# Performance work log

Measured on AMD Instinct MI355X. Metric: run time of the kernel, lower is better.

The kernel has to match this reference:

```python
import jax, jax.numpy as jnp
import numpy as np

WS = 12
NUM_HEADS = 6
EPS = 1e-5


def _ln(x, w, b):
    mu = jnp.mean(x, axis=-1, keepdims=True)
    var = jnp.var(x, axis=-1, keepdims=True)
    return (x - mu) * jax.lax.rsqrt(var + EPS) * w + b


def _lin(x, w, b):
    return jnp.einsum('...i,oi->...o', x, w) + b


def _window_partition(x, ws):
    # x: [B, C, H, W] -> [B*Nh*Nw, ws*ws, C]
    B, C, H, W = x.shape
    x = x.reshape(B, C, H // ws, ws, W // ws, ws)
    x = jnp.transpose(x, (0, 2, 4, 3, 5, 1))
    return x.reshape(-1, ws * ws, C)


def _window_reverse(win, ws, B, C, H, W):
    Nh, Nw = H // ws, W // ws
    x = win.reshape(B, Nh, Nw, ws, ws, C)
    x = jnp.transpose(x, (0, 5, 1, 3, 2, 4))
    return x.reshape(B, C, H, W)


def setup_inputs() -> dict:
    key = jax.random.key(0)
    ks = jax.random.split(key, 12)
    B, C, H, W = 4, 192, 240, 240
    hid = 4 * C
    s = 0.02
    return {
        'opt': jax.random.normal(ks[0], (B, C, H, W), jnp.float32),
        'sar': jax.random.normal(ks[1], (B, C, H, W), jnp.float32),
        'ln_q_w': jnp.ones((C,), jnp.float32), 'ln_q_b': jnp.zeros((C,), jnp.float32),
        'ln_kv_w': jnp.ones((C,), jnp.float32), 'ln_kv_b': jnp.zeros((C,), jnp.float32),
        'wq': jax.random.normal(ks[2], (C, C), jnp.float32) * s, 'bq': jnp.zeros((C,), jnp.float32),
        'wk': jax.random.normal(ks[3], (C, C), jnp.float32) * s, 'bk': jnp.zeros((C,), jnp.float32),
        'wv': jax.random.normal(ks[4], (C, C), jnp.float32) * s, 'bv': jnp.zeros((C,), jnp.float32),
        'wp': jax.random.normal(ks[5], (C, C), jnp.float32) * s, 'bp': jnp.zeros((C,), jnp.float32),
        'gw1': jax.random.normal(ks[6], (C, C), jnp.float32) * s, 'gb1': jnp.zeros((C,), jnp.float32),
        'gw2': jax.random.normal(ks[7], (C, C), jnp.float32) * s, 'gb2': jnp.zeros((C,), jnp.float32),
        'gamma': jnp.float32(0.1),
        'ln_o_w': jnp.ones((C,), jnp.float32), 'ln_o_b': jnp.zeros((C,), jnp.float32),
        'w1': jax.random.normal(ks[8], (hid, C), jnp.float32) * s, 'b1': jnp.zeros((hid,), jnp.float32),
        'w2': jax.random.normal(ks[9], (C, hid), jnp.float32) * s, 'b2': jnp.zeros((C,), jnp.float32),
    }


def reference(opt, sar, ln_q_w, ln_q_b, ln_kv_w, ln_kv_b, wq, bq, wk, bk, wv, bv,
              wp, bp, gw1, gb1, gw2, gb2, gamma, ln_o_w, ln_o_b, w1, b1, w2, b2):
    B, C, H, W = opt.shape
    Hh = NUM_HEADS
    hd = C // Hh
    scale = hd ** -0.5

    opt_tok = _window_partition(opt, WS)   # [Bn, N, C]
    sar_tok = _window_partition(sar, WS)
    Bn, N, _ = opt_tok.shape

    opt_ln = _ln(opt_tok, ln_q_w, ln_q_b)
    sar_ln = _ln(sar_tok, ln_kv_w, ln_kv_b)

    q = _lin(opt_ln, wq, bq).reshape(Bn, N, Hh, hd)
    k = _lin(sar_ln, wk, bk).reshape(Bn, N, Hh, hd)
    v = _lin(sar_ln, wv, bv).reshape(Bn, N, Hh, hd)

    attn = jnp.einsum('bnhd,bmhd->bhnm', q, k) * scale
    attn = jax.nn.softmax(attn, axis=-1)
    out = jnp.einsum('bhnm,bmhd->bnhd', attn, v).reshape(Bn, N, C)
    fused = _lin(out, wp, bp)

    # sigmoid gate on mean-pooled sar tokens
    g = jax.nn.sigmoid(_lin(jax.nn.gelu(_lin(jnp.mean(sar_ln, axis=1), gw1, gb1), approximate=False), gw2, gb2))
    fused = opt_tok + gamma * (g[:, None, :] * fused)

    h = _ln(fused, ln_o_w, ln_o_b)
    h = _lin(jax.nn.gelu(_lin(h, w1, b1), approximate=False), w2, b2)
    fused = fused + h

    return _window_reverse(fused, WS, B, C, H, W)
```

## Files before the change

### kernel.cpp

```cpp
#include <hip/hip_runtime.h>
#include <hip/hip_bf16.h>

#define ROWS 230400
#define CDIM 192
#define NTOK 144
#define NWIN 1600
#define PLANE 57600
#define HDIM 768

typedef __attribute__((ext_vector_type(8))) short bf16x8;
typedef __attribute__((ext_vector_type(4))) float f32x4;

__device__ __forceinline__ ushort f2bf(float f) {
  union { float f; unsigned u; } v; v.f = f;
  unsigned r = v.u + 0x7FFFu + ((v.u >> 16) & 1u);
  return (ushort)(r >> 16);
}
__device__ __forceinline__ float bf2f(ushort h) {
  union { unsigned u; float f; } v; v.u = ((unsigned)h) << 16;
  return v.f;
}
__device__ __forceinline__ float gelu_f(float x) {
  return 0.5f * x * (1.f + erff(x * 0.7071067811865475f));
}

struct CvtJobs {
  const float* src[8];
  ushort* dst[8];
  int n[8];
};
__global__ __launch_bounds__(256) void cvt_kernel(CvtJobs jobs) {
  int stride = gridDim.x * blockDim.x;
  int t0 = blockIdx.x * blockDim.x + threadIdx.x;
  for (int j = 0; j < 8; ++j) {
    const float* s = jobs.src[j]; ushort* d = jobs.dst[j]; int n = jobs.n[j];
    for (int e = t0; e < n; e += stride) d[e] = f2bf(s[e]);
  }
}

__global__ __launch_bounds__(256) void lnpart_kernel(
    const float* __restrict__ opt, const float* __restrict__ sar,
    const float* __restrict__ lnqw, const float* __restrict__ lnqb,
    const float* __restrict__ lnkw, const float* __restrict__ lnkb,
    ushort* __restrict__ opt_ln, ushort* __restrict__ sar_ln,
    ushort* __restrict__ opt_tok) {
  __shared__ __align__(16) ushort X[NTOK * 200];
  __shared__ float smu[NTOK], srs[NTOK];
  int win = blockIdx.x;
  int b = win / 400, rr = win % 400, nh = rr / 20, nw = rr % 20;
  size_t wbase = (size_t)b * CDIM * PLANE + (size_t)(nh * 12) * 240 + nw * 12;
  int tid = threadIdx.x;
  for (int pass = 0; pass < 2; ++pass) {
    const float* src = pass ? sar : opt;
    for (int e = tid; e < CDIM * 36; e += 256) {
      int c = e / 36, r2 = e % 36, i = r2 / 3, j0 = (r2 % 3) * 4;
      float4 v = *(const float4*)&src[wbase + (size_t)c * PLANE + i * 240 + j0];
      int tok = i * 12 + j0;
      X[(tok + 0) * 200 + c] = f2bf(v.x);
      X[(tok + 1) * 200 + c] = f2bf(v.y);
      X[(tok + 2) * 200 + c] = f2bf(v.z);
      X[(tok + 3) * 200 + c] = f2bf(v.w);
    }
    __syncthreads();
    if (tid < NTOK) {
      float s = 0.f, qs = 0.f;
      for (int c = 0; c < CDIM; ++c) { float v = bf2f(X[tid * 200 + c]); s += v; qs += v * v; }
      float mu = s * (1.f / CDIM);
      smu[tid] = mu;
      srs[tid] = rsqrtf(qs * (1.f / CDIM) - mu * mu + 1e-5f);
    }
    __syncthreads();
    const float* w = pass ? lnkw : lnqw;
    const float* bb = pass ? lnkb : lnqb;
    ushort* dst = pass ? sar_ln : opt_ln;
    for (int e = tid; e < NTOK * CDIM; e += 256) {
      int tok = e / CDIM, c = e % CDIM;
      ushort raw = X[tok * 200 + c];
      float v = bf2f(raw);
      float y = (v - smu[tok]) * srs[tok] * w[c] + bb[c];
      size_t o = (size_t)(win * NTOK + tok) * CDIM + c;
      dst[o] = f2bf(y);
      if (!pass) opt_tok[o] = raw;
    }
    __syncthreads();
  }
}

enum { EPI_BF16 = 0, EPI_GELU = 1, EPI_SIG = 2, EPI_PROJ = 3 };

template <int EPI>
__global__ __launch_bounds__(256) void gemm_kernel(
    const ushort* __restrict__ A, const ushort* __restrict__ Wt,
    const float* __restrict__ bias, const float* __restrict__ bias2,
    void* __restrict__ outp, int M, int N, int K,
    const float* __restrict__ g, const ushort* __restrict__ opt_tok,
    const float* __restrict__ gamma_p) {
  __shared__ __align__(16) ushort Alds[128 * 40];
  int m0 = blockIdx.x * 128;
  int n0 = blockIdx.y * 64;
  int tid = threadIdx.x;
  int wave = tid >> 6, lane = tid & 63, ls = lane & 15, quad = lane >> 4;
  f32x4 acc[2][4] = {};
  for (int k0 = 0; k0 < K; k0 += 32) {
    for (int it = 0; it < 2; ++it) {
      int ch = tid + 256 * it;
      int r = ch >> 2, c8 = (ch & 3) * 8;
      int grow = m0 + r; if (grow > M - 1) grow = M - 1;
      *(bf16x8*)&Alds[r * 40 + c8] = *(const bf16x8*)&A[(size_t)grow * K + k0 + c8];
    }
    __syncthreads();
    int mb = wave * 32;
    bf16x8 af0 = *(const bf16x8*)&Alds[(mb + ls) * 40 + quad * 8];
    bf16x8 af1 = *(const bf16x8*)&Alds[(mb + 16 + ls) * 40 + quad * 8];
    bf16x8 bfr[4];
    for (int nf = 0; nf < 4; ++nf)
      bfr[nf] = *(const bf16x8*)&Wt[(size_t)(n0 + nf * 16 + ls) * K + k0 + quad * 8];
    for (int nf = 0; nf < 4; ++nf) {
      acc[0][nf] = __builtin_amdgcn_mfma_f32_16x16x32_bf16(af0, bfr[nf], acc[0][nf], 0, 0, 0);
      acc[1][nf] = __builtin_amdgcn_mfma_f32_16x16x32_bf16(af1, bfr[nf], acc[1][nf], 0, 0, 0);
    }
    __syncthreads();
  }
  float gam = (EPI == EPI_PROJ) ? gamma_p[0] : 0.f;
  for (int s = 0; s < 2; ++s) {
    int rowbase = m0 + wave * 32 + s * 16 + quad * 4;
    for (int nf = 0; nf < 4; ++nf) {
      int col = n0 + nf * 16 + ls;
      float bb = (col < 192) ? bias[col] : bias2[col - 192];
      for (int r = 0; r < 4; ++r) {
        int row = rowbase + r;
        if (row >= M) continue;
        float v = acc[s][nf][r] + bb;
        if (EPI == EPI_BF16) {
          ((ushort*)outp)[(size_t)row * N + col] = f2bf(v);
        } else if (EPI == EPI_GELU) {
          ((ushort*)outp)[(size_t)row * N + col] = f2bf(gelu_f(v));
        } else if (EPI == EPI_SIG) {
          ((float*)outp)[(size_t)row * N + col] = 1.f / (1.f + __expf(-v));
        } else {
          int win = row / NTOK;
          float gv = g[(size_t)win * CDIM + col];
          float ov = bf2f(opt_tok[(size_t)row * CDIM + col]);
          ((ushort*)outp)[(size_t)row * CDIM + col] = f2bf(ov + gam * gv * v);
        }
      }
    }
  }
}

__global__ __launch_bounds__(192) void pool_kernel(const ushort* __restrict__ sar_ln,
                                                   ushort* __restrict__ pool) {
  int win = blockIdx.x, c = threadIdx.x;
  float s = 0.f;
  size_t base = (size_t)win * NTOK * CDIM + c;
  for (int t = 0; t < NTOK; ++t) s += bf2f(sar_ln[base + (size_t)t * CDIM]);
  pool[(size_t)win * CDIM + c] = f2bf(s * (1.f / NTOK));
}

__global__ __launch_bounds__(256) void attn_kernel(const ushort* __restrict__ q,
                                                   const ushort* __restrict__ kv,
                                                   ushort* __restrict__ attn_out) {
  __shared__ __align__(16) ushort vT[32 * 168];
  __shared__ __align__(16) ushort P[4][16 * 168];
  int blk = blockIdx.x;
  int win = blk / 6, head = blk % 6;
  int tid = threadIdx.x, wave = tid >> 6, lane = tid & 63, ls = lane & 15, quad = lane >> 4;
  size_t qbase = (size_t)win * NTOK * CDIM + head * 32;
  size_t kbase = (size_t)win * NTOK * 384 + head * 32;
  size_t vbase = kbase + 192;
  for (int e = tid; e < NTOK * 32; e += 256) {
    int t = e >> 5, d = e & 31;
    vT[d * 168 + t] = kv[vbase + (size_t)t * 384 + d];
  }
  for (int e = tid; e < 32 * 24; e += 256) {
    int d = e / 24, j = 144 + e % 24;
    vT[d * 168 + j] = 0;
  }
  __syncthreads();
  const float scale = 0.17677669529663687f;
  ushort* Pw = P[wave];
  f32x4 zero = {0.f, 0.f, 0.f, 0.f};
  for (int mt = wave; mt < 9; mt += 4) {
    int m0 = mt * 16;
    bf16x8 aq = *(const bf16x8*)&q[qbase + (size_t)(m0 + ls) * CDIM + quad * 8];
    f32x4 S[9];
    for (int nt = 0; nt < 9; ++nt) {
      bf16x8 bk = *(const bf16x8*)&kv[kbase + (size_t)(nt * 16 + ls) * 384 + quad * 8];
      S[nt] = __builtin_amdgcn_mfma_f32_16x16x32_bf16(aq, bk, zero, 0, 0, 0);
    }
    for (int nt = 0; nt < 9; ++nt)
      for (int r = 0; r < 4; ++r) S[nt][r] *= scale;
    for (int r = 0; r < 4; ++r) {
      float mx = -1e30f;
      for (int nt = 0; nt < 9; ++nt) mx = fmaxf(mx, S[nt][r]);
      for (int o = 1; o < 16; o <<= 1) mx = fmaxf(mx, __shfl_xor(mx, o));
      float sm = 0.f;
      for (int nt = 0; nt < 9; ++nt) { float e = __expf(S[nt][r] - mx); S[nt][r] = e; sm += e; }
      for (int o = 1; o < 16; o <<= 1) sm += __shfl_xor(sm, o);
      float inv = 1.f / sm;
      for (int nt = 0; nt < 9; ++nt)
        Pw[(quad * 4 + r) * 168 + nt * 16 + ls] = f2bf(S[nt][r] * inv);
    }
    for (int e = lane; e < 16 * 24; e += 64) {
      int r = e / 24, j = 144 + e % 24;
      Pw[r * 168 + j] = 0;
    }
    f32x4 O[2] = {};
    for (int ks = 0; ks < 5; ++ks) {
      bf16x8 ap = *(const bf16x8*)&Pw[ls * 168 + ks * 32 + quad * 8];
      for (int dt = 0; dt < 2; ++dt) {
        bf16x8 bv = *(const bf16x8*)&vT[(dt * 16 + ls) * 168 + ks * 32 + quad * 8];
        O[dt] = __builtin_amdgcn_mfma_f32_16x16x32_bf16(ap, bv, O[dt], 0, 0, 0);
      }
    }
    for (int dt = 0; dt < 2; ++dt)
      for (int r = 0; r < 4; ++r)
        attn_out[(size_t)(win * NTOK + m0 + quad * 4 + r) * CDIM + head * 32 + dt * 16 + ls] =
            f2bf(O[dt][r]);
  }
}

__global__ __launch_bounds__(256) void lno_kernel(const ushort* __restrict__ x,
                                                  const float* __restrict__ w,
                                                  const float* __restrict__ b,
                                                  ushort* __restrict__ out) {
  int row = blockIdx.x * 4 + (threadIdx.x >> 6);
  int lane = threadIdx.x & 63;
  const ushort* xr = x + (size_t)row * CDIM;
  float v[3], s = 0.f, qs = 0.f;
  for (int i = 0; i < 3; ++i) { v[i] = bf2f(xr[lane + 64 * i]); s += v[i]; qs += v[i] * v[i]; }
  for (int o = 1; o < 64; o <<= 1) { s += __shfl_xor(s, o); qs += __shfl_xor(qs, o); }
  float mu = s * (1.f / CDIM);
  float rs = rsqrtf(qs * (1.f / CDIM) - mu * mu + 1e-5f);
  ushort* orow = out + (size_t)row * CDIM;
  for (int i = 0; i < 3; ++i) {
    int c = lane + 64 * i;
    orow[c] = f2bf((v[i] - mu) * rs * w[c] + b[c]);
  }
}

__global__ __launch_bounds__(256, 2) void mlp_kernel(
    const ushort* __restrict__ h, const ushort* __restrict__ fused,
    const ushort* __restrict__ w1b, const float* __restrict__ b1,
    const ushort* __restrict__ w2b, const float* __restrict__ b2,
    ushort* __restrict__ y) {
  __shared__ __align__(16) ushort Hs[128 * 200];
  __shared__ __align__(16) ushort Ts[128 * 72];
  int m0 = blockIdx.x * 128;
  int tid = threadIdx.x, wave = tid >> 6, lane = tid & 63, ls = lane & 15, quad = lane >> 4;
  for (int it = 0; it < 12; ++it) {
    int ch = tid + 256 * it;
    int r = ch / 24, c8 = (ch % 24) * 8;
    *(bf16x8*)&Hs[r * 200 + c8] = *(const bf16x8*)&h[(size_t)(m0 + r) * CDIM + c8];
  }
  __syncthreads();
  int mb = wave * 32;
  f32x4 acc[2][12] = {};
  for (int hc = 0; hc < HDIM; hc += 64) {
    f32x4 t[2][4] = {};
    for (int ks = 0; ks < 6; ++ks) {
      bf16x8 a0 = *(const bf16x8*)&Hs[(mb + ls) * 200 + ks * 32 + quad * 8];
      bf16x8 a1 = *(const bf16x8*)&Hs[(mb + 16 + ls) * 200 + ks * 32 + quad * 8];
      for (int nf = 0; nf < 4; ++nf) {
        bf16x8 bw = *(const bf16x8*)&w1b[(size_t)(hc + nf * 16 + ls) * CDIM + ks * 32 + quad * 8];
        t[0][nf] = __builtin_amdgcn_mfma_f32_16x16x32_bf16(a0, bw, t[0][nf], 0, 0, 0);
        t[1][nf] = __builtin_amdgcn_mfma_f32_16x16x32_bf16(a1, bw, t[1][nf], 0, 0, 0);
      }
    }
    for (int s = 0; s < 2; ++s)
      for (int nf = 0; nf < 4; ++nf) {
        float bb = b1[hc + nf * 16 + ls];
        for (int r = 0; r < 4; ++r) {
          float v = gelu_f(t[s][nf][r] + bb);
          Ts[(mb + s * 16 + quad * 4 + r) * 72 + nf * 16 + ls] = f2bf(v);
        }
      }
    for (int ks = 0; ks < 2; ++ks) {
      bf16x8 a0 = *(const bf16x8*)&Ts[(mb + ls) * 72 + ks * 32 + quad * 8];
      bf16x8 a1 = *(const bf16x8*)&Ts[(mb + 16 + ls) * 72 + ks * 32 + quad * 8];
      for (int nf = 0; nf < 12; ++nf) {
        bf16x8 bw = *(const bf16x8*)&w2b[(size_t)(nf * 16 + ls) * HDIM + hc + ks * 32 + quad * 8];
        acc[0][nf] = __builtin_amdgcn_mfma_f32_16x16x32_bf16(a0, bw, acc[0][nf], 0, 0, 0);
        acc[1][nf] = __builtin_amdgcn_mfma_f32_16x16x32_bf16(a1, bw, acc[1][nf], 0, 0, 0);
      }
    }
  }
  for (int s = 0; s < 2; ++s)
    for (int nf = 0; nf < 12; ++nf) {
      float bb = b2[nf * 16 + ls];
      for (int r = 0; r < 4; ++r) {
        size_t idx = (size_t)(m0 + mb + s * 16 + quad * 4 + r) * CDIM + nf * 16 + ls;
        y[idx] = f2bf(bf2f(fused[idx]) + acc[s][nf][r] + bb);
      }
    }
}

__global__ __launch_bounds__(256) void unpart_kernel(const ushort* __restrict__ y,
                                                     float* __restrict__ out) {
  __shared__ __align__(16) ushort X[NTOK * 200];
  int win = blockIdx.x;
  int b = win / 400, rr = win % 400, nh = rr / 20, nw = rr % 20;
  size_t wbase = (size_t)b * CDIM * PLANE + (size_t)(nh * 12) * 240 + nw * 12;
  int tid = threadIdx.x;
  for (int e = tid; e < NTOK * 24; e += 256) {
    int tok = e / 24, c8 = (e % 24) * 8;
    *(bf16x8*)&X[tok * 200 + c8] = *(const bf16x8*)&y[(size_t)(win * NTOK + tok) * CDIM + c8];
  }
  __syncthreads();
  for (int e = tid; e < CDIM * 36; e += 256) {
    int c = e / 36, r2 = e % 36, i = r2 / 3, j0 = (r2 % 3) * 4;
    int tok = i * 12 + j0;
    float4 v;
    v.x = bf2f(X[(tok + 0) * 200 + c]);
    v.y = bf2f(X[(tok + 1) * 200 + c]);
    v.z = bf2f(X[(tok + 2) * 200 + c]);
    v.w = bf2f(X[(tok + 3) * 200 + c]);
    *(float4*)&out[wbase + (size_t)c * PLANE + i * 240 + j0] = v;
  }
}

extern "C" void kernel_launch(void* const* d_in, const int* in_sizes, int n_in,
                              void* d_out, int out_size, void* d_ws, size_t ws_size,
                              hipStream_t stream) {
  const float* opt   = (const float*)d_in[0];
  const float* sar   = (const float*)d_in[1];
  const float* lnqw  = (const float*)d_in[2];
  const float* lnqb  = (const float*)d_in[3];
  const float* lnkw  = (const float*)d_in[4];
  const float* lnkb  = (const float*)d_in[5];
  const float* wq    = (const float*)d_in[6];
  const float* bq    = (const float*)d_in[7];
  const float* wk    = (const float*)d_in[8];
  const float* bk    = (const float*)d_in[9];
  const float* wv    = (const float*)d_in[10];
  const float* bv    = (const float*)d_in[11];
  const float* wp    = (const float*)d_in[12];
  const float* bp    = (const float*)d_in[13];
  const float* gw1   = (const float*)d_in[14];
  const float* gb1   = (const float*)d_in[15];
  const float* gw2   = (const float*)d_in[16];
  const float* gb2   = (const float*)d_in[17];
  const float* gamma = (const float*)d_in[18];
  const float* lnow  = (const float*)d_in[19];
  const float* lnob  = (const float*)d_in[20];
  const float* w1    = (const float*)d_in[21];
  const float* b1    = (const float*)d_in[22];
  const float* w2    = (const float*)d_in[23];
  const float* b2    = (const float*)d_in[24];

  char* ws = (char*)d_ws;
  size_t off = 0;
  auto take = [&](size_t bytes) -> char* {
    char* p = ws + off;
    off += (bytes + 255) & ~(size_t)255;
    return p;
  };
  const size_t big = (size_t)ROWS * CDIM * 2;
  ushort* opt_ln  = (ushort*)take(big);
  ushort* sar_ln  = (ushort*)take(big);
  ushort* opt_tok = (ushort*)take(big);
  ushort* qb      = (ushort*)take(big);
  ushort* kv      = (ushort*)take((size_t)ROWS * 384 * 2);
  ushort* wq_bf   = (ushort*)take(CDIM * CDIM * 2);
  ushort* wkv_bf  = (ushort*)take(2 * CDIM * CDIM * 2);
  ushort* wp_bf   = (ushort*)take(CDIM * CDIM * 2);
  ushort* w1_bf   = (ushort*)take((size_t)HDIM * CDIM * 2);
  ushort* w2_bf   = (ushort*)take((size_t)CDIM * HDIM * 2);
  ushort* gw1_bf  = (ushort*)take(CDIM * CDIM * 2);
  ushort* gw2_bf  = (ushort*)take(CDIM * CDIM * 2);
  ushort* pool_bf = (ushort*)take(NWIN * CDIM * 2);
  ushort* g1_bf   = (ushort*)take(NWIN * CDIM * 2);
  float*  g_f     = (float*)take(NWIN * CDIM * 4);
  ushort* h        = opt_ln;
  ushort* attn_out = sar_ln;
  ushort* fused    = qb;
  ushort* yb       = sar_ln;

  CvtJobs jobs;
  jobs.src[0] = wq;  jobs.dst[0] = wq_bf;               jobs.n[0] = CDIM * CDIM;
  jobs.src[1] = wk;  jobs.dst[1] = wkv_bf;              jobs.n[1] = CDIM * CDIM;
  jobs.src[2] = wv;  jobs.dst[2] = wkv_bf + CDIM * CDIM; jobs.n[2] = CDIM * CDIM;
  jobs.src[3] = wp;  jobs.dst[3] = wp_bf;               jobs.n[3] = CDIM * CDIM;
  jobs.src[4] = w1;  jobs.dst[4] = w1_bf;               jobs.n[4] = HDIM * CDIM;
  jobs.src[5] = w2;  jobs.dst[5] = w2_bf;               jobs.n[5] = CDIM * HDIM;
  jobs.src[6] = gw1; jobs.dst[6] = gw1_bf;              jobs.n[6] = CDIM * CDIM;
  jobs.src[7] = gw2; jobs.dst[7] = gw2_bf;              jobs.n[7] = CDIM * CDIM;
  cvt_kernel<<<dim3(128), dim3(256), 0, stream>>>(jobs);

  lnpart_kernel<<<dim3(NWIN), dim3(256), 0, stream>>>(
      opt, sar, lnqw, lnqb, lnkw, lnkb, opt_ln, sar_ln, opt_tok);

  gemm_kernel<EPI_BF16><<<dim3(1800, 3), dim3(256), 0, stream>>>(
      opt_ln, wq_bf, bq, bq, (void*)qb, ROWS, CDIM, CDIM, nullptr, nullptr, nullptr);
  gemm_kernel<EPI_BF16><<<dim3(1800, 6), dim3(256), 0, stream>>>(
      sar_ln, wkv_bf, bk, bv, (void*)kv, ROWS, 384, CDIM, nullptr, nullptr, nullptr);

  pool_kernel<<<dim3(NWIN), dim3(192), 0, stream>>>(sar_ln, pool_bf);
  gemm_kernel<EPI_GELU><<<dim3(13, 3), dim3(256), 0, stream>>>(
      pool_bf, gw1_bf, gb1, gb1, (void*)g1_bf, NWIN, CDIM, CDIM, nullptr, nullptr, nullptr);
  gemm_kernel<EPI_SIG><<<dim3(13, 3), dim3(256), 0, stream>>>(
      g1_bf, gw2_bf, gb2, gb2, (void*)g_f, NWIN, CDIM, CDIM, nullptr, nullptr, nullptr);

  attn_kernel<<<dim3(NWIN * 6), dim3(256), 0, stream>>>(qb, kv, attn_out);

  gemm_kernel<EPI_PROJ><<<dim3(1800, 3), dim3(256), 0, stream>>>(
      attn_out, wp_bf, bp, bp, (void*)fused, ROWS, CDIM, CDIM, g_f, opt_tok, gamma);

  lno_kernel<<<dim3(ROWS / 4), dim3(256), 0, stream>>>(fused, lnow, lnob, h);

  mlp_kernel<<<dim3(1800), dim3(256), 0, stream>>>(h, fused, w1_bf, b1, w2_bf, b2, yb);

  unpart_kernel<<<dim3(NWIN), dim3(256), 0, stream>>>(yb, (float*)d_out);
}
```

Measured before the change: 2.274 ms.

## Shrink MLP tile to 64 rows per block with register-held A fragments

The fused MLP kernel drops from 128 to 64 rows per block, with each wave handling 16 rows instead of 32. The input activations are loaded straight into registers as MFMA A fragments instead of being staged through shared memory, which removes the large Hs buffer and the barrier. Launch bounds rise to 4 blocks per CU for more occupancy. In exchange, every weight fragment loaded from global memory now feeds one MFMA instead of two, so weight traffic per FLOP doubles.

Result: slower. 2.758 ms (+21.2%).

```diff
diff --git a/kernel.cpp b/kernel.cpp
--- a/kernel.cpp
+++ b/kernel.cpp
@@ -239,60 +239,58 @@
   }
 }
 
-__global__ __launch_bounds__(256, 2) void mlp_kernel(
+__global__ __launch_bounds__(256, 4) void mlp_kernel(
     const ushort* __restrict__ h, const ushort* __restrict__ fused,
     const ushort* __restrict__ w1b, const float* __restrict__ b1,
     const ushort* __restrict__ w2b, const float* __restrict__ b2,
     ushort* __restrict__ y) {
-  __shared__ __align__(16) ushort Hs[128 * 200];
-  __shared__ __align__(16) ushort Ts[128 * 72];
-  int m0 = blockIdx.x * 128;
+  __shared__ __align__(16) ushort Ts[64 * 72];
+  int m0 = blockIdx.x * 64;
   int tid = threadIdx.x, wave = tid >> 6, lane = tid & 63, ls = lane & 15, quad = lane >> 4;
-  for (int it = 0; it < 12; ++it) {
-    int ch = tid + 256 * it;
-    int r = ch / 24, c8 = (ch % 24) * 8;
-    *(bf16x8*)&Hs[r * 200 + c8] = *(const bf16x8*)&h[(size_t)(m0 + r) * CDIM + c8];
-  }
-  __syncthreads();
-  int mb = wave * 32;
-  f32x4 acc[2][12] = {};
+  int wrow = wave * 16;
+  bf16x8 afrag[6];
+#pragma unroll
+  for (int ks = 0; ks < 6; ++ks)
+    afrag[ks] = *(const bf16x8*)&h[(size_t)(m0 + wrow + ls) * CDIM + ks * 32 + quad * 8];
+  f32x4 acc[12] = {};
   for (int hc = 0; hc < HDIM; hc += 64) {
-    f32x4 t[2][4] = {};
+    f32x4 t[4] = {};
+#pragma unroll
     for (int ks = 0; ks < 6; ++ks) {
-      bf16x8 a0 = *(const bf16x8*)&Hs[(mb + ls) * 200 + ks * 32 + quad * 8];
-      bf16x8 a1 = *(const bf16x8*)&Hs[(mb + 16 + ls) * 200 + ks * 32 + quad * 8];
+#pragma unroll
       for (int nf = 0; nf < 4; ++nf) {
         bf16x8 bw = *(const bf16x8*)&w1b[(size_t)(hc + nf * 16 + ls) * CDIM + ks * 32 + quad * 8];
-        t[0][nf] = __builtin_amdgcn_mfma_f32_16x16x32_bf16(a0, bw, t[0][nf], 0, 0, 0);
-        t[1][nf] = __builtin_amdgcn_mfma_f32_16x16x32_bf16(a1, bw, t[1][nf], 0, 0, 0);
+        t[nf] = __builtin_amdgcn_mfma_f32_16x16x32_bf16(afrag[ks], bw, t[nf], 0, 0, 0);
       }
     }
-    for (int s = 0; s < 2; ++s)
-      for (int nf = 0; nf < 4; ++nf) {
-        float bb = b1[hc + nf * 16 + ls];
-        for (int r = 0; r < 4; ++r) {
-          float v = gelu_f(t[s][nf][r] + bb);
-          Ts[(mb + s * 16 + quad * 4 + r) * 72 + nf * 16 + ls] = f2bf(v);
-        }
+#pragma unroll
+    for (int nf = 0; nf < 4; ++nf) {
+      float bb = b1[hc + nf * 16 + ls];
+#pragma unroll
+      for (int r = 0; r < 4; ++r) {
+        float v = gelu_f(t[nf][r] + bb);
+        Ts[(wrow + quad * 4 + r) * 72 + nf * 16 + ls] = f2bf(v);
       }
+    }
+#pragma unroll
     for (int ks = 0; ks < 2; ++ks) {
-      bf16x8 a0 = *(const bf16x8*)&Ts[(mb + ls) * 72 + ks * 32 + quad * 8];
-      bf16x8 a1 = *(const bf16x8*)&Ts[(mb + 16 + ls) * 72 + ks * 32 + quad * 8];
+      bf16x8 ap = *(const bf16x8*)&Ts[(wrow + ls) * 72 + ks * 32 + quad * 8];
+#pragma unroll
       for (int nf = 0; nf < 12; ++nf) {
         bf16x8 bw = *(const bf16x8*)&w2b[(size_t)(nf * 16 + ls) * HDIM + hc + ks * 32 + quad * 8];
-        acc[0][nf] = __builtin_amdgcn_mfma_f32_16x16x32_bf16(a0, bw, acc[0][nf], 0, 0, 0);
-        acc[1][nf] = __builtin_amdgcn_mfma_f32_16x16x32_bf16(a1, bw, acc[1][nf], 0, 0, 0);
+        acc[nf] = __builtin_amdgcn_mfma_f32_16x16x32_bf16(ap, bw, acc[nf], 0, 0, 0);
       }
     }
   }
-  for (int s = 0; s < 2; ++s)
-    for (int nf = 0; nf < 12; ++nf) {
-      float bb = b2[nf * 16 + ls];
-      for (int r = 0; r < 4; ++r) {
-        size_t idx = (size_t)(m0 + mb + s * 16 + quad * 4 + r) * CDIM + nf * 16 + ls;
-        y[idx] = f2bf(bf2f(fused[idx]) + acc[s][nf][r] + bb);
-      }
-    }
+#pragma unroll
+  for (int nf = 0; nf < 12; ++nf) {
+    float bb = b2[nf * 16 + ls];
+#pragma unroll
+    for (int r = 0; r < 4; ++r) {
+      size_t idx = (size_t)(m0 + wrow + quad * 4 + r) * CDIM + nf * 16 + ls;
+      y[idx] = f2bf(bf2f(fused[idx]) + acc[nf][r] + bb);
+    }
+  }
 }
 
 __global__ __launch_bounds__(256) void unpart_kernel(const ushort* __restrict__ y,
@@ -408,7 +406,7 @@
 
   lno_kernel<<<dim3(ROWS / 4), dim3(256), 0, stream>>>(fused, lnow, lnob, h);
 
-  mlp_kernel<<<dim3(1800), dim3(256), 0, stream>>>(h, fused, w1_bf, b1, w2_bf, b2, yb);
+  mlp_kernel<<<dim3(ROWS / 64), dim3(256), 0, stream>>>(h, fused, w1_bf, b1, w2_bf, b2, yb);
 
   unpart_kernel<<<dim3(NWIN), dim3(256), 0, stream>>>(yb, (float*)d_out);
 }
```
